# Kernel tuning notes

Hardware: AMD Instinct MI355X
Metric: run time of the kernel (lower is better)

Reference implementation:

```python
import jax, jax.numpy as jnp
import numpy as np

B, N, F = 4, 4096, 32
NG = 14  # number of gate graph-convs in GCNLSTM_Cell with memory state


def setup_inputs() -> dict:
    key = jax.random.key(0)
    ks = jax.random.split(key, 7)
    x = jax.random.normal(ks[0], (B, N, F), jnp.float32)
    h = jax.random.normal(ks[1], (B, N, F), jnp.float32)
    c = jax.random.normal(ks[2], (B, N, F), jnp.float32)
    m = jax.random.normal(ks[3], (B, N, F), jnp.float32)
    # weighted dense adjacency, scaled so row sums are O(1)
    adj = jax.random.uniform(ks[4], (N, N), jnp.float32) / N
    # 14 WeightedGraphConv layers: Dense F -> 2F (single FeedForward layer, no relu)
    W = jax.random.normal(ks[5], (NG, F, 2 * F), jnp.float32) * (1.0 / np.sqrt(F))
    b = jnp.zeros((NG, 2 * F), jnp.float32)
    return {"x": x, "h": h, "c": c, "m": m, "adj": adj, "W": W, "b": b}


def _gcn(ax, W, b):
    # ax: [B,N,F] = adj @ state (precomputed); Dense to 2F then GLU split.
    z = ax @ W + b  # [B,N,2F]
    ls, rs = jnp.split(z, 2, axis=-1)
    return ls * jax.nn.sigmoid(rs)


def reference(x, h, c, m, adj, W, b):
    # shared graph aggregation for x and h (adj is the same for all gates)
    ax = jnp.einsum('nm,bmf->bnf', adj, x)  # [B,N,F]
    ah = jnp.einsum('nm,bmf->bnf', adj, h)

    fx = _gcn(ax, W[0], b[0]); fh = _gcn(ah, W[1], b[1])
    ix = _gcn(ax, W[2], b[2]); ih = _gcn(ah, W[3], b[3])
    cx = _gcn(ax, W[4], b[4]); ch = _gcn(ah, W[5], b[5])
    ox = _gcn(ax, W[6], b[6]); oh = _gcn(ah, W[7], b[7])

    f = jax.nn.sigmoid(fx + fh)
    i = jax.nn.sigmoid(ix + ih)
    o = jax.nn.sigmoid(ox + oh)
    c_new = f * c + i * jnp.tanh(cx + ch)
    h1 = o * jnp.tanh(c_new)

    # memory-state block (6 more graph convs on h1 and m)
    ah1 = jnp.einsum('nm,bmf->bnf', adj, h1)
    am = jnp.einsum('nm,bmf->bnf', adj, m)
    sa_ih = _gcn(ah1, W[8], b[8]);  sa_im = _gcn(am, W[9], b[9])
    sa_gh = _gcn(ah1, W[10], b[10]); sa_gm = _gcn(am, W[11], b[11])
    sa_oh = _gcn(ah1, W[12], b[12]); sa_om = _gcn(am, W[13], b[13])

    i2 = jax.nn.sigmoid(sa_ih + sa_im)
    g = jax.nn.sigmoid(sa_gh + sa_gm)
    o2 = jax.nn.sigmoid(sa_oh + sa_om)
    m_new = i2 * m + (1.0 - i2) * g
    h_new = m_new * o2
    return h_new, c_new, m_new
```

## Files before the change

kernel.cpp:

```cpp
#include <hip/hip_runtime.h>
#include <stdint.h>

typedef __attribute__((ext_vector_type(4))) float f32x4;
typedef __attribute__((ext_vector_type(8))) short s16x8;

#define BB 4
#define NN 4096
#define FF 32
#define BNF (BB*NN*FF)

static __device__ __forceinline__ float bf2f(uint16_t u) {
    union { uint32_t i; float f; } v; v.i = ((uint32_t)u) << 16; return v.f;
}
static __device__ __forceinline__ uint16_t f2bf(float f) {
    union { float f; uint32_t i; } v; v.f = f;
    uint32_t r = v.i + 0x7FFFu + ((v.i >> 16) & 1u);
    return (uint16_t)(r >> 16);
}
static __device__ __forceinline__ float sig_acc(float x) { return 1.0f / (1.0f + expf(-x)); }

__global__ __launch_bounds__(256) void cvt_adj(const float* __restrict__ a,
                                               uint16_t* __restrict__ ab)
{
    size_t i = ((size_t)blockIdx.x * 256 + threadIdx.x) * 8;
    float4 v0 = *(const float4*)(a + i);
    float4 v1 = *(const float4*)(a + i + 4);
    union { uint4 u; uint16_t e[8]; } o;
    o.e[0] = f2bf(v0.x); o.e[1] = f2bf(v0.y); o.e[2] = f2bf(v0.z); o.e[3] = f2bf(v0.w);
    o.e[4] = f2bf(v1.x); o.e[5] = f2bf(v1.y); o.e[6] = f2bf(v1.z); o.e[7] = f2bf(v1.w);
    *(uint4*)(ab + i) = o.u;
}

__global__ __launch_bounds__(256) void pack_kernel(
    const float* __restrict__ s0, const float* __restrict__ s1,
    uint16_t* __restrict__ dst)
{
    int bid = blockIdx.x;
    int tensor = bid >> 8;
    int b = (bid >> 6) & 3;
    int ntile = bid & 63;
    const float* src = tensor ? s1 : s0;
    int n0 = ntile * 64;
    __shared__ uint16_t tl[32][65];
    int t = threadIdx.x;
    {
        int i = t >> 2, ch = t & 3;
        size_t idx = ((size_t)(b * NN + n0 + i)) * FF + ch * 8;
        float4 v0 = *(const float4*)(src + idx);
        float4 v1 = *(const float4*)(src + idx + 4);
        uint16_t e[8] = { f2bf(v0.x), f2bf(v0.y), f2bf(v0.z), f2bf(v0.w),
                          f2bf(v1.x), f2bf(v1.y), f2bf(v1.z), f2bf(v1.w) };
        #pragma unroll
        for (int k = 0; k < 8; k++) tl[ch * 8 + k][i] = e[k];
    }
    __syncthreads();
    {
        int f = t >> 3, ch = t & 7;
        union { uint4 u; uint16_t e[8]; } v;
        #pragma unroll
        for (int k = 0; k < 8; k++) v.e[k] = tl[f][ch * 8 + k];
        size_t row = (size_t)(tensor * 128 + b * 32 + f);
        *(uint4*)(dst + row * NN + n0 + ch * 8) = v.u;
    }
}

__global__ __launch_bounds__(256) void gemm_kernel(
    const void* __restrict__ Av,
    const uint16_t* __restrict__ Bt,
    float* __restrict__ part, uint16_t* __restrict__ Cb,
    int kLen, int direct, int isf32A)
{
    int mt = blockIdx.x, nt = blockIdx.y, ks = blockIdx.z;
    int m0 = mt * 128, c0 = nt * 128, k0 = ks * kLen;
    __shared__ __align__(16) uint16_t aL[128 * 32];
    __shared__ __align__(16) uint16_t bL[128 * 32];
    int t = threadIdx.x;
    int lane = t & 63, w = t >> 6;
    int wm = (w & 1) * 64, wn = (w >> 1) * 64;
    int lm = lane & 15, lk = lane >> 4;

    const uint16_t* A16 = (const uint16_t*)Av;
    const float*    Af  = (const float*)Av;

    f32x4 acc[4][4] = {};

    for (int kk = k0; kk < k0 + kLen; kk += 32) {
        union { uint4 u; uint16_t e[8]; } sa[2], sb[2];
        #pragma unroll
        for (int q = 0; q < 2; q++) {
            int pos = q * 4096 + t * 16;
            int row = pos >> 6;
            int col = (pos & 63) >> 1;
            size_t aidx = (size_t)(m0 + row) * 4096 + kk + col;
            size_t bidx = (size_t)(c0 + row) * 4096 + kk + col;
            if (!isf32A) {
                sa[q].u = *(const uint4*)(A16 + aidx);
            } else {
                union { uint4 u[2]; float f[8]; } va;
                va.u[0] = *(const uint4*)(Af + aidx);
                va.u[1] = *(const uint4*)(Af + aidx + 4);
                #pragma unroll
                for (int k = 0; k < 8; k++) sa[q].e[k] = f2bf(va.f[k]);
            }
            sb[q].u = *(const uint4*)(Bt + bidx);
        }
        #pragma unroll
        for (int q = 0; q < 2; q++) {
            int pos = q * 4096 + t * 16;
            *(uint4*)((char*)aL + pos) = sa[q].u;
            *(uint4*)((char*)bL + pos) = sb[q].u;
        }
        __syncthreads();
        s16x8 af[4], bfr[4];
        #pragma unroll
        for (int i = 0; i < 4; i++)
            af[i] = *(const s16x8*)(aL + (wm + i * 16 + lm) * 32 + lk * 8);
        #pragma unroll
        for (int j = 0; j < 4; j++)
            bfr[j] = *(const s16x8*)(bL + (wn + j * 16 + lm) * 32 + lk * 8);
        #pragma unroll
        for (int i = 0; i < 4; i++)
            #pragma unroll
            for (int j = 0; j < 4; j++)
                acc[i][j] = __builtin_amdgcn_mfma_f32_16x16x32_bf16(af[i], bfr[j], acc[i][j], 0, 0, 0);
        __syncthreads();
    }

    int r4 = (lane >> 4) * 4;
    if (direct) {
        #pragma unroll
        for (int i = 0; i < 4; i++)
            #pragma unroll
            for (int j = 0; j < 4; j++) {
                int c = c0 + wn + j * 16 + lm;
                int mr = m0 + wm + i * 16 + r4;
                union { uint2 u; uint16_t e[4]; } v;
                #pragma unroll
                for (int r = 0; r < 4; r++) v.e[r] = f2bf(acc[i][j][r]);
                *(uint2*)(Cb + (size_t)c * 4096 + mr) = v.u;
            }
    } else {
        #pragma unroll
        for (int i = 0; i < 4; i++)
            #pragma unroll
            for (int j = 0; j < 4; j++) {
                int c = c0 + wn + j * 16 + lm;
                int mr = m0 + wm + i * 16 + r4;
                *(f32x4*)(part + ((size_t)ks * 256 + c) * 4096 + mr) = acc[i][j];
            }
    }
}

__global__ __launch_bounds__(256) void reduce_kernel(
    const float* __restrict__ part, uint16_t* __restrict__ out, int ns)
{
    int idx = blockIdx.x * 256 + threadIdx.x;
    size_t base = (size_t)idx * 4;
    f32x4 s = {};
    for (int k = 0; k < ns; k++)
        s += *(const f32x4*)(part + (size_t)k * (256 * 4096) + base);
    union { uint2 u; uint16_t e[4]; } v;
    #pragma unroll
    for (int k = 0; k < 4; k++) v.e[k] = f2bf(s[k]);
    *(uint2*)(out + base) = v.u;
}

__global__ __launch_bounds__(256) void fuse1_kernel(
    const uint16_t* __restrict__ C1,
    const float* __restrict__ Wf, const float* __restrict__ bf_,
    const float* __restrict__ cf,
    float* __restrict__ cnew, uint16_t* __restrict__ S2t)
{
    __shared__ uint32_t WL[8 * 32 * 32];
    __shared__ float BL[8 * 64];
    __shared__ float AL[32][65];
    __shared__ uint16_t H1[32][33];

    int t = threadIdx.x;
    int bid = blockIdx.x;
    int b = bid >> 7, ntile = bid & 127;
    int n0 = ntile * 32;

    for (int i = t; i < 8192; i += 256) {
        int g = i >> 10, rem = i & 1023, f = rem >> 5, j = rem & 31;
        uint32_t lo = f2bf(Wf[g * 2048 + f * 64 + j]);
        uint32_t hi = f2bf(Wf[g * 2048 + f * 64 + 32 + j]);
        WL[i] = lo | (hi << 16);
    }
    if (t < 128) {
        #pragma unroll
        for (int k = 0; k < 4; k++) BL[t * 4 + k] = bf_[t * 4 + k];
    }
    {
        int r = t >> 2, ch = t & 3;
        size_t crow = (r < 32) ? (size_t)(b * 32 + r) : (size_t)(128 + b * 32 + (r - 32));
        union { uint4 u; uint16_t e[8]; } v;
        v.u = *(const uint4*)(C1 + crow * 4096 + n0 + ch * 8);
        #pragma unroll
        for (int k = 0; k < 8; k++) AL[ch * 8 + k][r] = bf2f(v.e[k]);
    }
    __syncthreads();

    int j = t & 31, nb = t >> 5;
    float acc[4][16];
    #pragma unroll
    for (int u = 0; u < 4; u++)
        #pragma unroll
        for (int g = 0; g < 8; g++) {
            acc[u][g * 2]     = BL[g * 64 + j];
            acc[u][g * 2 + 1] = BL[g * 64 + 32 + j];
        }
    #pragma unroll 2
    for (int f = 0; f < 32; f++) {
        float wls[8], wrs[8];
        #pragma unroll
        for (int g = 0; g < 8; g++) {
            uint32_t wv = WL[g * 1024 + f * 32 + j];
            wls[g] = __uint_as_float(wv << 16);
            wrs[g] = __uint_as_float(wv & 0xFFFF0000u);
        }
        #pragma unroll
        for (int u = 0; u < 4; u++) {
            int node = nb + u * 8;
            float ax = AL[node][f], ah = AL[node][32 + f];
            #pragma unroll
            for (int g = 0; g < 8; g++) {
                float src = (g & 1) ? ah : ax;
                acc[u][g * 2]     += src * wls[g];
                acc[u][g * 2 + 1] += src * wrs[g];
            }
        }
    }
    #pragma unroll
    for (int u = 0; u < 4; u++) {
        int node = nb + u * 8;
        float fx = acc[u][0]  * sig_acc(acc[u][1]);
        float fh = acc[u][2]  * sig_acc(acc[u][3]);
        float ix = acc[u][4]  * sig_acc(acc[u][5]);
        float ih = acc[u][6]  * sig_acc(acc[u][7]);
        float cx = acc[u][8]  * sig_acc(acc[u][9]);
        float ch = acc[u][10] * sig_acc(acc[u][11]);
        float ox = acc[u][12] * sig_acc(acc[u][13]);
        float oh = acc[u][14] * sig_acc(acc[u][15]);
        float fg = sig_acc(fx + fh), ig = sig_acc(ix + ih), og = sig_acc(ox + oh);
        size_t gidx = ((size_t)(b * NN + n0 + node)) * FF + j;
        float cvv = cf[gidx];
        float cn = fg * cvv + ig * tanhf(cx + ch);
        float h1 = og * tanhf(cn);
        cnew[gidx] = cn;
        H1[j][node] = f2bf(h1);
    }
    __syncthreads();
    {
        int fr = t >> 3, ch = t & 7;
        union { uint2 u; uint16_t e[4]; } v;
        #pragma unroll
        for (int k = 0; k < 4; k++) v.e[k] = H1[fr][ch * 4 + k];
        *(uint2*)(S2t + ((size_t)(b * 32 + fr)) * NN + n0 + ch * 4) = v.u;
    }
}

__global__ __launch_bounds__(256) void fuse2_kernel(
    const uint16_t* __restrict__ C2,
    const float* __restrict__ Wf, const float* __restrict__ bf_,
    const float* __restrict__ mf,
    float* __restrict__ hnew, float* __restrict__ mnew)
{
    __shared__ uint32_t WL[6 * 32 * 32];
    __shared__ float BL[6 * 64];
    __shared__ float AL[32][65];

    int t = threadIdx.x;
    int bid = blockIdx.x;
    int b = bid >> 7, ntile = bid & 127;
    int n0 = ntile * 32;

    for (int i = t; i < 6144; i += 256) {
        int g = i >> 10, rem = i & 1023, f = rem >> 5, j = rem & 31;
        int gg = 8 + g;
        uint32_t lo = f2bf(Wf[gg * 2048 + f * 64 + j]);
        uint32_t hi = f2bf(Wf[gg * 2048 + f * 64 + 32 + j]);
        WL[i] = lo | (hi << 16);
    }
    if (t < 96) {
        #pragma unroll
        for (int k = 0; k < 4; k++) BL[t * 4 + k] = bf_[512 + t * 4 + k];
    }
    {
        int r = t >> 2, ch = t & 3;
        size_t crow = (r < 32) ? (size_t)(b * 32 + r) : (size_t)(128 + b * 32 + (r - 32));
        union { uint4 u; uint16_t e[8]; } v;
        v.u = *(const uint4*)(C2 + crow * 4096 + n0 + ch * 8);
        #pragma unroll
        for (int k = 0; k < 8; k++) AL[ch * 8 + k][r] = bf2f(v.e[k]);
    }
    __syncthreads();

    int j = t & 31, nb = t >> 5;
    float acc[4][12];
    #pragma unroll
    for (int u = 0; u < 4; u++)
        #pragma unroll
        for (int g = 0; g < 6; g++) {
            acc[u][g * 2]     = BL[g * 64 + j];
            acc[u][g * 2 + 1] = BL[g * 64 + 32 + j];
        }
    #pragma unroll 2
    for (int f = 0; f < 32; f++) {
        float wls[6], wrs[6];
        #pragma unroll
        for (int g = 0; g < 6; g++) {
            uint32_t wv = WL[g * 1024 + f * 32 + j];
            wls[g] = __uint_as_float(wv << 16);
            wrs[g] = __uint_as_float(wv & 0xFFFF0000u);
        }
        #pragma unroll
        for (int u = 0; u < 4; u++) {
            int node = nb + u * 8;
            float ah1 = AL[node][f], am = AL[node][32 + f];
            #pragma unroll
            for (int g = 0; g < 6; g++) {
                float src = (g & 1) ? am : ah1;
                acc[u][g * 2]     += src * wls[g];
                acc[u][g * 2 + 1] += src * wrs[g];
            }
        }
    }
    #pragma unroll
    for (int u = 0; u < 4; u++) {
        int node = nb + u * 8;
        float sa_ih = acc[u][0]  * sig_acc(acc[u][1]);
        float sa_im = acc[u][2]  * sig_acc(acc[u][3]);
        float sa_gh = acc[u][4]  * sig_acc(acc[u][5]);
        float sa_gm = acc[u][6]  * sig_acc(acc[u][7]);
        float sa_oh = acc[u][8]  * sig_acc(acc[u][9]);
        float sa_om = acc[u][10] * sig_acc(acc[u][11]);
        float i2 = sig_acc(sa_ih + sa_im);
        float g2 = sig_acc(sa_gh + sa_gm);
        float o2 = sig_acc(sa_oh + sa_om);
        size_t gidx = ((size_t)(b * NN + n0 + node)) * FF + j;
        float mvv = mf[gidx];
        float mn = i2 * mvv + (1.0f - i2) * g2;
        float hn = mn * o2;
        mnew[gidx] = mn;
        hnew[gidx] = hn;
    }
}

extern "C" void kernel_launch(void* const* d_in, const int* in_sizes, int n_in,
                              void* d_out, int out_size, void* d_ws, size_t ws_size,
                              hipStream_t stream) {
    (void)in_sizes; (void)n_in; (void)out_size;
    const float* x   = (const float*)d_in[0];
    const float* h   = (const float*)d_in[1];
    const float* c   = (const float*)d_in[2];
    const float* m   = (const float*)d_in[3];
    const float* adj = (const float*)d_in[4];
    const float* W   = (const float*)d_in[5];
    const float* bb  = (const float*)d_in[6];
    float* out = (float*)d_out;

    char* ws = (char*)d_ws;
    int haveAdjb = ws_size >= (size_t)(36u << 20);
    uint16_t* adjb = (uint16_t*)ws;
    size_t pOff = haveAdjb ? (size_t)(32u << 20) : 0;
    uint16_t* P    = (uint16_t*)(ws + pOff);
    uint16_t* Cbuf = (uint16_t*)(ws + pOff + (2u << 20));
    size_t partOff = pOff + (4u << 20);
    float* part = (float*)(ws + partOff);

    if (ws_size < (4u << 20)) return;
    size_t avail = ws_size - partOff;
    int ns = 0;
    if      (avail >= (size_t)(32u << 20)) ns = 8;
    else if (avail >= (size_t)(16u << 20)) ns = 4;
    else if (avail >= (size_t)( 8u << 20)) ns = 2;
    else if (avail >= (size_t)( 4u << 20)) ns = 1;

    const void* Agemm = haveAdjb ? (const void*)adjb : (const void*)adj;
    int isf32A = haveAdjb ? 0 : 1;

    if (haveAdjb) cvt_adj<<<8192, 256, 0, stream>>>(adj, adjb);

    pack_kernel<<<512, 256, 0, stream>>>(x, h, P);
    if (ns) {
        gemm_kernel<<<dim3(32, 2, ns), 256, 0, stream>>>(Agemm, P, part, nullptr, 4096 / ns, 0, isf32A);
        reduce_kernel<<<1024, 256, 0, stream>>>(part, Cbuf, ns);
    } else {
        gemm_kernel<<<dim3(32, 2, 1), 256, 0, stream>>>(Agemm, P, nullptr, Cbuf, 4096, 1, isf32A);
    }
    fuse1_kernel<<<512, 256, 0, stream>>>(Cbuf, W, bb, c, out + BNF, P);
    pack_kernel<<<256, 256, 0, stream>>>(m, m, P + (size_t)128 * NN);
    if (ns) {
        gemm_kernel<<<dim3(32, 2, ns), 256, 0, stream>>>(Agemm, P, part, nullptr, 4096 / ns, 0, isf32A);
        reduce_kernel<<<1024, 256, 0, stream>>>(part, Cbuf, ns);
    } else {
        gemm_kernel<<<dim3(32, 2, 1), 256, 0, stream>>>(Agemm, P, nullptr, Cbuf, 4096, 1, isf32A);
    }
    fuse2_kernel<<<512, 256, 0, stream>>>(Cbuf, W, bb, m, out, out + 2 * BNF);
}
```

Measured before the change: 210.1 us.

## Fuse split-K reduction into gate kernels and use MFMA for gate dense layers

Removes the separate split-K reduce kernels by having the fused gate kernels sum the fp32 partials directly while loading their tiles. The per-gate dense F->2F projections now run on bf16 MFMA instructions instead of scalar FMAs. Weights are pre-converted once into a swizzled bf16 layout by a new prep kernel, replacing the per-block conversion. Tiles grow to 64 nodes, so half as many blocks are launched. The cost is an extra bf16 rounding of the aggregated activations and a larger workspace requirement.

```diff
diff --git a/kernel.cpp b/kernel.cpp
--- a/kernel.cpp
+++ b/kernel.cpp
@@ -29,6 +29,20 @@
     o.e[0] = f2bf(v0.x); o.e[1] = f2bf(v0.y); o.e[2] = f2bf(v0.z); o.e[3] = f2bf(v0.w);
     o.e[4] = f2bf(v1.x); o.e[5] = f2bf(v1.y); o.e[6] = f2bf(v1.z); o.e[7] = f2bf(v1.w);
     *(uint4*)(ab + i) = o.u;
+}
+
+__global__ __launch_bounds__(256) void prep_w(const float* __restrict__ Wf,
+                                              uint16_t* __restrict__ Wp)
+{
+    int idx = blockIdx.x * 256 + threadIdx.x;
+    int g   = idx >> 11;
+    int k   = (idx >> 6) & 31;
+    int col = idx & 63;
+    uint16_t v = f2bf(Wf[idx]);
+    int gp = g >> 1;
+    int sl = ((g & 1) << 2) | (k >> 3);
+    int ph = sl ^ (col & 7);
+    Wp[((gp * 64 + col) * 64) + ph * 8 + (k & 7)] = v;
 }
 
 __global__ __launch_bounds__(256) void pack_kernel(
@@ -151,200 +165,255 @@
     }
 }
 
-__global__ __launch_bounds__(256) void reduce_kernel(
-    const float* __restrict__ part, uint16_t* __restrict__ out, int ns)
-{
-    int idx = blockIdx.x * 256 + threadIdx.x;
-    size_t base = (size_t)idx * 4;
-    f32x4 s = {};
-    for (int k = 0; k < ns; k++)
-        s += *(const f32x4*)(part + (size_t)k * (256 * 4096) + base);
-    union { uint2 u; uint16_t e[4]; } v;
-    #pragma unroll
-    for (int k = 0; k < 4; k++) v.e[k] = f2bf(s[k]);
-    *(uint2*)(out + base) = v.u;
-}
-
 __global__ __launch_bounds__(256) void fuse1_kernel(
-    const uint16_t* __restrict__ C1,
-    const float* __restrict__ Wf, const float* __restrict__ bf_,
+    const float* __restrict__ part,
+    const uint16_t* __restrict__ Cbi,
+    const uint16_t* __restrict__ Wp,
+    const float* __restrict__ bf_,
     const float* __restrict__ cf,
-    float* __restrict__ cnew, uint16_t* __restrict__ S2t)
-{
-    __shared__ uint32_t WL[8 * 32 * 32];
-    __shared__ float BL[8 * 64];
-    __shared__ float AL[32][65];
-    __shared__ uint16_t H1[32][33];
+    float* __restrict__ cnew, uint16_t* __restrict__ S2t, int ns)
+{
+    __shared__ __align__(16) uint16_t WL[4 * 64 * 64];
+    __shared__ __align__(16) float    AL[64 * 68];
+    __shared__ __align__(16) float    BL[512];
+    __shared__ __align__(16) uint16_t H1[32 * 72];
 
     int t = threadIdx.x;
-    int bid = blockIdx.x;
-    int b = bid >> 7, ntile = bid & 127;
-    int n0 = ntile * 32;
-
-    for (int i = t; i < 8192; i += 256) {
-        int g = i >> 10, rem = i & 1023, f = rem >> 5, j = rem & 31;
-        uint32_t lo = f2bf(Wf[g * 2048 + f * 64 + j]);
-        uint32_t hi = f2bf(Wf[g * 2048 + f * 64 + 32 + j]);
-        WL[i] = lo | (hi << 16);
-    }
-    if (t < 128) {
-        #pragma unroll
-        for (int k = 0; k < 4; k++) BL[t * 4 + k] = bf_[t * 4 + k];
-    }
+    int b = blockIdx.x >> 6, n0 = (blockIdx.x & 63) * 64;
+
+    {
+        const uint4* src = (const uint4*)Wp;
+        uint4* dst = (uint4*)WL;
+        #pragma unroll
+        for (int i = 0; i < 8; i++) dst[t + i * 256] = src[t + i * 256];
+    }
+    if (t < 128) *(float4*)(BL + t * 4) = *(const float4*)(bf_ + t * 4);
+
     {
         int r = t >> 2, ch = t & 3;
         size_t crow = (r < 32) ? (size_t)(b * 32 + r) : (size_t)(128 + b * 32 + (r - 32));
-        union { uint4 u; uint16_t e[8]; } v;
-        v.u = *(const uint4*)(C1 + crow * 4096 + n0 + ch * 8);
-        #pragma unroll
-        for (int k = 0; k < 8; k++) AL[ch * 8 + k][r] = bf2f(v.e[k]);
+        f32x4 a0, a1, a2, a3;
+        if (ns) {
+            const float* s0p = part + crow * 4096 + n0 + ch * 16;
+            a0 = *(const f32x4*)(s0p);
+            a1 = *(const f32x4*)(s0p + 4);
+            a2 = *(const f32x4*)(s0p + 8);
+            a3 = *(const f32x4*)(s0p + 12);
+            for (int ks = 1; ks < ns; ks++) {
+                const float* sp = s0p + (size_t)ks * (256 * 4096);
+                a0 += *(const f32x4*)(sp);
+                a1 += *(const f32x4*)(sp + 4);
+                a2 += *(const f32x4*)(sp + 8);
+                a3 += *(const f32x4*)(sp + 12);
+            }
+        } else {
+            const uint16_t* cp = Cbi + crow * 4096 + n0 + ch * 16;
+            union { uint4 u; uint16_t e[8]; } v0, v1;
+            v0.u = *(const uint4*)(cp);
+            v1.u = *(const uint4*)(cp + 8);
+            #pragma unroll
+            for (int k = 0; k < 4; k++) {
+                a0[k] = bf2f(v0.e[k]);     a1[k] = bf2f(v0.e[4 + k]);
+                a2[k] = bf2f(v1.e[k]);     a3[k] = bf2f(v1.e[4 + k]);
+            }
+        }
+        float* al = AL + r * 68 + ch * 16;
+        *(f32x4*)(al) = a0; *(f32x4*)(al + 4) = a1;
+        *(f32x4*)(al + 8) = a2; *(f32x4*)(al + 12) = a3;
     }
     __syncthreads();
 
-    int j = t & 31, nb = t >> 5;
-    float acc[4][16];
-    #pragma unroll
-    for (int u = 0; u < 4; u++)
-        #pragma unroll
-        for (int g = 0; g < 8; g++) {
-            acc[u][g * 2]     = BL[g * 64 + j];
-            acc[u][g * 2 + 1] = BL[g * 64 + 32 + j];
-        }
-    #pragma unroll 2
-    for (int f = 0; f < 32; f++) {
-        float wls[8], wrs[8];
-        #pragma unroll
-        for (int g = 0; g < 8; g++) {
-            uint32_t wv = WL[g * 1024 + f * 32 + j];
-            wls[g] = __uint_as_float(wv << 16);
-            wrs[g] = __uint_as_float(wv & 0xFFFF0000u);
-        }
-        #pragma unroll
-        for (int u = 0; u < 4; u++) {
-            int node = nb + u * 8;
-            float ax = AL[node][f], ah = AL[node][32 + f];
-            #pragma unroll
-            for (int g = 0; g < 8; g++) {
-                float src = (g & 1) ? ah : ax;
-                acc[u][g * 2]     += src * wls[g];
-                acc[u][g * 2 + 1] += src * wrs[g];
-            }
-        }
-    }
-    #pragma unroll
-    for (int u = 0; u < 4; u++) {
-        int node = nb + u * 8;
-        float fx = acc[u][0]  * sig_acc(acc[u][1]);
-        float fh = acc[u][2]  * sig_acc(acc[u][3]);
-        float ix = acc[u][4]  * sig_acc(acc[u][5]);
-        float ih = acc[u][6]  * sig_acc(acc[u][7]);
-        float cx = acc[u][8]  * sig_acc(acc[u][9]);
-        float ch = acc[u][10] * sig_acc(acc[u][11]);
-        float ox = acc[u][12] * sig_acc(acc[u][13]);
-        float oh = acc[u][14] * sig_acc(acc[u][15]);
-        float fg = sig_acc(fx + fh), ig = sig_acc(ix + ih), og = sig_acc(ox + oh);
-        size_t gidx = ((size_t)(b * NN + n0 + node)) * FF + j;
-        float cvv = cf[gidx];
-        float cn = fg * cvv + ig * tanhf(cx + ch);
-        float h1 = og * tanhf(cn);
-        cnew[gidx] = cn;
-        H1[j][node] = f2bf(h1);
+    int lane = t & 63, w = t >> 6;
+    int j = lane & 15, kg = lane >> 4;
+    int r4 = kg * 4;
+
+    float cv[2][4];
+    #pragma unroll
+    for (int h = 0; h < 2; h++)
+        #pragma unroll
+        for (int r = 0; r < 4; r++)
+            cv[h][r] = cf[((size_t)(b * NN + n0 + w * 16 + r4 + r)) * FF + j + h * 16];
+
+    s16x8 a_ax, a_ah;
+    {
+        int col = w * 16 + j;
+        #pragma unroll
+        for (int e = 0; e < 8; e++) {
+            int k = kg * 8 + e;
+            a_ax[e] = (short)f2bf(AL[k * 68 + col]);
+            a_ah[e] = (short)f2bf(AL[(32 + k) * 68 + col]);
+        }
+    }
+
+    float s[4][2][4];
+    #pragma unroll
+    for (int p = 0; p < 4; p++) {
+        int g0 = p * 2, g1 = p * 2 + 1;
+        f32x4 ac0[4] = {}, ac1[4] = {};
+        #pragma unroll
+        for (int ct = 0; ct < 4; ct++) {
+            int col = ct * 16 + j;
+            int ph0 = (kg)     ^ (col & 7);
+            int ph1 = (4 + kg) ^ (col & 7);
+            s16x8 b0 = *(const s16x8*)(WL + (p * 64 + col) * 64 + ph0 * 8);
+            s16x8 b1 = *(const s16x8*)(WL + (p * 64 + col) * 64 + ph1 * 8);
+            ac0[ct] = __builtin_amdgcn_mfma_f32_16x16x32_bf16(a_ax, b0, ac0[ct], 0, 0, 0);
+            ac1[ct] = __builtin_amdgcn_mfma_f32_16x16x32_bf16(a_ah, b1, ac1[ct], 0, 0, 0);
+        }
+        #pragma unroll
+        for (int h = 0; h < 2; h++)
+            #pragma unroll
+            for (int r = 0; r < 4; r++) {
+                float z0l = ac0[h][r]     + BL[g0 * 64 + h * 16 + j];
+                float z0r = ac0[2 + h][r] + BL[g0 * 64 + 32 + h * 16 + j];
+                float z1l = ac1[h][r]     + BL[g1 * 64 + h * 16 + j];
+                float z1r = ac1[2 + h][r] + BL[g1 * 64 + 32 + h * 16 + j];
+                s[p][h][r] = z0l * sig_acc(z0r) + z1l * sig_acc(z1r);
+            }
+    }
+
+    #pragma unroll
+    for (int h = 0; h < 2; h++) {
+        union { uint2 u; uint16_t e[4]; } pk;
+        #pragma unroll
+        for (int r = 0; r < 4; r++) {
+            size_t gidx = ((size_t)(b * NN + n0 + w * 16 + r4 + r)) * FF + j + h * 16;
+            float fg = sig_acc(s[0][h][r]);
+            float ig = sig_acc(s[1][h][r]);
+            float cc = tanhf(s[2][h][r]);
+            float og = sig_acc(s[3][h][r]);
+            float cn = fg * cv[h][r] + ig * cc;
+            cnew[gidx] = cn;
+            pk.e[r] = f2bf(og * tanhf(cn));
+        }
+        *(uint2*)(H1 + (j + h * 16) * 72 + w * 16 + r4) = pk.u;
     }
     __syncthreads();
     {
         int fr = t >> 3, ch = t & 7;
-        union { uint2 u; uint16_t e[4]; } v;
-        #pragma unroll
-        for (int k = 0; k < 4; k++) v.e[k] = H1[fr][ch * 4 + k];
-        *(uint2*)(S2t + ((size_t)(b * 32 + fr)) * NN + n0 + ch * 4) = v.u;
+        uint4 v = *(const uint4*)(H1 + fr * 72 + ch * 8);
+        *(uint4*)(S2t + ((size_t)(b * 32 + fr)) * NN + n0 + ch * 8) = v;
     }
 }
 
 __global__ __launch_bounds__(256) void fuse2_kernel(
-    const uint16_t* __restrict__ C2,
-    const float* __restrict__ Wf, const float* __restrict__ bf_,
+    const float* __restrict__ part,
+    const uint16_t* __restrict__ Cbi,
+    const uint16_t* __restrict__ Wp,
+    const float* __restrict__ bf_,
     const float* __restrict__ mf,
-    float* __restrict__ hnew, float* __restrict__ mnew)
-{
-    __shared__ uint32_t WL[6 * 32 * 32];
-    __shared__ float BL[6 * 64];
-    __shared__ float AL[32][65];
+    float* __restrict__ hnew, float* __restrict__ mnew, int ns)
+{
+    __shared__ __align__(16) uint16_t WL[3 * 64 * 64];
+    __shared__ __align__(16) float    AL[64 * 68];
+    __shared__ __align__(16) float    BL[384];
 
     int t = threadIdx.x;
-    int bid = blockIdx.x;
-    int b = bid >> 7, ntile = bid & 127;
-    int n0 = ntile * 32;
-
-    for (int i = t; i < 6144; i += 256) {
-        int g = i >> 10, rem = i & 1023, f = rem >> 5, j = rem & 31;
-        int gg = 8 + g;
-        uint32_t lo = f2bf(Wf[gg * 2048 + f * 64 + j]);
-        uint32_t hi = f2bf(Wf[gg * 2048 + f * 64 + 32 + j]);
-        WL[i] = lo | (hi << 16);
-    }
-    if (t < 96) {
-        #pragma unroll
-        for (int k = 0; k < 4; k++) BL[t * 4 + k] = bf_[512 + t * 4 + k];
-    }
+    int b = blockIdx.x >> 6, n0 = (blockIdx.x & 63) * 64;
+
+    {
+        const uint4* src = (const uint4*)(Wp + 4 * 64 * 64);
+        uint4* dst = (uint4*)WL;
+        #pragma unroll
+        for (int i = 0; i < 6; i++) dst[t + i * 256] = src[t + i * 256];
+    }
+    if (t < 96) *(float4*)(BL + t * 4) = *(const float4*)(bf_ + 512 + t * 4);
+
     {
         int r = t >> 2, ch = t & 3;
         size_t crow = (r < 32) ? (size_t)(b * 32 + r) : (size_t)(128 + b * 32 + (r - 32));
-        union { uint4 u; uint16_t e[8]; } v;
-        v.u = *(const uint4*)(C2 + crow * 4096 + n0 + ch * 8);
-        #pragma unroll
-        for (int k = 0; k < 8; k++) AL[ch * 8 + k][r] = bf2f(v.e[k]);
+        f32x4 a0, a1, a2, a3;
+        if (ns) {
+            const float* s0p = part + crow * 4096 + n0 + ch * 16;
+            a0 = *(const f32x4*)(s0p);
+            a1 = *(const f32x4*)(s0p + 4);
+            a2 = *(const f32x4*)(s0p + 8);
+            a3 = *(const f32x4*)(s0p + 12);
+            for (int ks = 1; ks < ns; ks++) {
+                const float* sp = s0p + (size_t)ks * (256 * 4096);
+                a0 += *(const f32x4*)(sp);
+                a1 += *(const f32x4*)(sp + 4);
+                a2 += *(const f32x4*)(sp + 8);
+                a3 += *(const f32x4*)(sp + 12);
+            }
+        } else {
+            const uint16_t* cp = Cbi + crow * 4096 + n0 + ch * 16;
+            union { uint4 u; uint16_t e[8]; } v0, v1;
+            v0.u = *(const uint4*)(cp);
+            v1.u = *(const uint4*)(cp + 8);
+            #pragma unroll
+            for (int k = 0; k < 4; k++) {
+                a0[k] = bf2f(v0.e[k]);     a1[k] = bf2f(v0.e[4 + k]);
+                a2[k] = bf2f(v1.e[k]);     a3[k] = bf2f(v1.e[4 + k]);
+            }
+        }
+        float* al = AL + r * 68 + ch * 16;
+        *(f32x4*)(al) = a0; *(f32x4*)(al + 4) = a1;
+        *(f32x4*)(al + 8) = a2; *(f32x4*)(al + 12) = a3;
     }
     __syncthreads();
 
-    int j = t & 31, nb = t >> 5;
-    float acc[4][12];
-    #pragma unroll
-    for (int u = 0; u < 4; u++)
-        #pragma unroll
-        for (int g = 0; g < 6; g++) {
-            acc[u][g * 2]     = BL[g * 64 + j];
-            acc[u][g * 2 + 1] = BL[g * 64 + 32 + j];
-        }
-    #pragma unroll 2
-    for (int f = 0; f < 32; f++) {
-        float wls[6], wrs[6];
-        #pragma unroll
-        for (int g = 0; g < 6; g++) {
-            uint32_t wv = WL[g * 1024 + f * 32 + j];
-            wls[g] = __uint_as_float(wv << 16);
-            wrs[g] = __uint_as_float(wv & 0xFFFF0000u);
-        }
-        #pragma unroll
-        for (int u = 0; u < 4; u++) {
-            int node = nb + u * 8;
-            float ah1 = AL[node][f], am = AL[node][32 + f];
-            #pragma unroll
-            for (int g = 0; g < 6; g++) {
-                float src = (g & 1) ? am : ah1;
-                acc[u][g * 2]     += src * wls[g];
-                acc[u][g * 2 + 1] += src * wrs[g];
-            }
-        }
-    }
-    #pragma unroll
-    for (int u = 0; u < 4; u++) {
-        int node = nb + u * 8;
-        float sa_ih = acc[u][0]  * sig_acc(acc[u][1]);
-        float sa_im = acc[u][2]  * sig_acc(acc[u][3]);
-        float sa_gh = acc[u][4]  * sig_acc(acc[u][5]);
-        float sa_gm = acc[u][6]  * sig_acc(acc[u][7]);
-        float sa_oh = acc[u][8]  * sig_acc(acc[u][9]);
-        float sa_om = acc[u][10] * sig_acc(acc[u][11]);
-        float i2 = sig_acc(sa_ih + sa_im);
-        float g2 = sig_acc(sa_gh + sa_gm);
-        float o2 = sig_acc(sa_oh + sa_om);
-        size_t gidx = ((size_t)(b * NN + n0 + node)) * FF + j;
-        float mvv = mf[gidx];
-        float mn = i2 * mvv + (1.0f - i2) * g2;
-        float hn = mn * o2;
-        mnew[gidx] = mn;
-        hnew[gidx] = hn;
-    }
+    int lane = t & 63, w = t >> 6;
+    int j = lane & 15, kg = lane >> 4;
+    int r4 = kg * 4;
+
+    float mv[2][4];
+    #pragma unroll
+    for (int h = 0; h < 2; h++)
+        #pragma unroll
+        for (int r = 0; r < 4; r++)
+            mv[h][r] = mf[((size_t)(b * NN + n0 + w * 16 + r4 + r)) * FF + j + h * 16];
+
+    s16x8 a_h1, a_m;
+    {
+        int col = w * 16 + j;
+        #pragma unroll
+        for (int e = 0; e < 8; e++) {
+            int k = kg * 8 + e;
+            a_h1[e] = (short)f2bf(AL[k * 68 + col]);
+            a_m[e]  = (short)f2bf(AL[(32 + k) * 68 + col]);
+        }
+    }
+
+    float s[3][2][4];
+    #pragma unroll
+    for (int p = 0; p < 3; p++) {
+        int g0 = p * 2, g1 = p * 2 + 1;
+        f32x4 ac0[4] = {}, ac1[4] = {};
+        #pragma unroll
+        for (int ct = 0; ct < 4; ct++) {
+            int col = ct * 16 + j;
+            int ph0 = (kg)     ^ (col & 7);
+            int ph1 = (4 + kg) ^ (col & 7);
+            s16x8 b0 = *(const s16x8*)(WL + (p * 64 + col) * 64 + ph0 * 8);
+            s16x8 b1 = *(const s16x8*)(WL + (p * 64 + col) * 64 + ph1 * 8);
+            ac0[ct] = __builtin_amdgcn_mfma_f32_16x16x32_bf16(a_h1, b0, ac0[ct], 0, 0, 0);
+            ac1[ct] = __builtin_amdgcn_mfma_f32_16x16x32_bf16(a_m, b1, ac1[ct], 0, 0, 0);
+        }
+        #pragma unroll
+        for (int h = 0; h < 2; h++)
+            #pragma unroll
+            for (int r = 0; r < 4; r++) {
+                float z0l = ac0[h][r]     + BL[g0 * 64 + h * 16 + j];
+                float z0r = ac0[2 + h][r] + BL[g0 * 64 + 32 + h * 16 + j];
+                float z1l = ac1[h][r]     + BL[g1 * 64 + h * 16 + j];
+                float z1r = ac1[2 + h][r] + BL[g1 * 64 + 32 + h * 16 + j];
+                s[p][h][r] = z0l * sig_acc(z0r) + z1l * sig_acc(z1r);
+            }
+    }
+
+    #pragma unroll
+    for (int h = 0; h < 2; h++)
+        #pragma unroll
+        for (int r = 0; r < 4; r++) {
+            size_t gidx = ((size_t)(b * NN + n0 + w * 16 + r4 + r)) * FF + j + h * 16;
+            float i2 = sig_acc(s[0][h][r]);
+            float gg = sig_acc(s[1][h][r]);
+            float o2 = sig_acc(s[2][h][r]);
+            float mn = i2 * mv[h][r] + (1.0f - i2) * gg;
+            mnew[gidx] = mn;
+            hnew[gidx] = mn * o2;
+        }
 }
 
 extern "C" void kernel_launch(void* const* d_in, const int* in_sizes, int n_in,
@@ -361,15 +430,16 @@
     float* out = (float*)d_out;
 
     char* ws = (char*)d_ws;
-    int haveAdjb = ws_size >= (size_t)(36u << 20);
+    int haveAdjb = ws_size >= (size_t)(40u << 20);
     uint16_t* adjb = (uint16_t*)ws;
     size_t pOff = haveAdjb ? (size_t)(32u << 20) : 0;
     uint16_t* P    = (uint16_t*)(ws + pOff);
     uint16_t* Cbuf = (uint16_t*)(ws + pOff + (2u << 20));
-    size_t partOff = pOff + (4u << 20);
+    uint16_t* Wp   = (uint16_t*)(ws + pOff + (4u << 20));
+    size_t partOff = pOff + (5u << 20);
     float* part = (float*)(ws + partOff);
 
-    if (ws_size < (4u << 20)) return;
+    if (ws_size < (6u << 20)) return;
     size_t avail = ws_size - partOff;
     int ns = 0;
     if      (avail >= (size_t)(32u << 20)) ns = 8;
@@ -381,21 +451,20 @@
     int isf32A = haveAdjb ? 0 : 1;
 
     if (haveAdjb) cvt_adj<<<8192, 256, 0, stream>>>(adj, adjb);
+    prep_w<<<112, 256, 0, stream>>>(W, Wp);
 
     pack_kernel<<<512, 256, 0, stream>>>(x, h, P);
     if (ns) {
         gemm_kernel<<<dim3(32, 2, ns), 256, 0, stream>>>(Agemm, P, part, nullptr, 4096 / ns, 0, isf32A);
-        reduce_kernel<<<1024, 256, 0, stream>>>(part, Cbuf, ns);
     } else {
         gemm_kernel<<<dim3(32, 2, 1), 256, 0, stream>>>(Agemm, P, nullptr, Cbuf, 4096, 1, isf32A);
     }
-    fuse1_kernel<<<512, 256, 0, stream>>>(Cbuf, W, bb, c, out + BNF, P);
+    fuse1_kernel<<<256, 256, 0, stream>>>(part, Cbuf, Wp, bb, c, out + BNF, P, ns);
     pack_kernel<<<256, 256, 0, stream>>>(m, m, P + (size_t)128 * NN);
     if (ns) {
         gemm_kernel<<<dim3(32, 2, ns), 256, 0, stream>>>(Agemm, P, part, nullptr, 4096 / ns, 0, isf32A);
-        reduce_kernel<<<1024, 256, 0, stream>>>(part, Cbuf, ns);
     } else {
         gemm_kernel<<<dim3(32, 2, 1), 256, 0, stream>>>(Agemm, P, nullptr, Cbuf, 4096, 1, isf32A);
     }
-    fuse2_kernel<<<512, 256, 0, stream>>>(Cbuf, W, bb, m, out, out + 2 * BNF);
-}
+    fuse2_kernel<<<256, 256, 0, stream>>>(part, Cbuf, Wp, bb, m, out, out + 2 * BNF, ns);
+}
```

Result: faster. 186.2 us (-11.3%).
